# Optimization experiments

Measured on AMD Instinct MI355X. Metric: run time of the kernel, lower is better.

Reference implementation:

```python
import jax, jax.numpy as jnp
import numpy as np

N, B, F_X, F_U, H, E = 1000000, 4096, 128, 128, 64, 1024


def setup_inputs() -> dict:
    key = jax.random.key(0)
    ks = jax.random.split(key, 12)
    scale = lambda fan_in: 1.0 / np.sqrt(fan_in)
    return {
        "x": jax.random.normal(ks[0], (N, F_X), dtype=jnp.float32),
        "edge_index": jax.random.randint(ks[1], (2, E), 0, N, dtype=jnp.int64),
        "e": jax.random.normal(ks[2], (E, 16), dtype=jnp.float32),
        "u": jax.random.normal(ks[3], (B, F_U), dtype=jnp.float32),
        "batch": jnp.sort(jax.random.randint(ks[4], (N,), 0, B, dtype=jnp.int64)),
        "Wk": jax.random.uniform(ks[5], (F_X, H), jnp.float32, -scale(F_X), scale(F_X)),
        "bk": jax.random.uniform(ks[6], (H,), jnp.float32, -scale(F_X), scale(F_X)),
        "Wq": jax.random.uniform(ks[7], (F_U, H), jnp.float32, -scale(F_U), scale(F_U)),
        "bq": jax.random.uniform(ks[8], (H,), jnp.float32, -scale(F_U), scale(F_U)),
        "Wu": jax.random.uniform(ks[9], (F_X + F_U, F_U), jnp.float32, -scale(F_X + F_U), scale(F_X + F_U)),
        "bu": jax.random.uniform(ks[10], (F_U,), jnp.float32, -scale(F_X + F_U), scale(F_X + F_U)),
    }


def reference(x, edge_index, e, u, batch, Wk, bk, Wq, bq, Wu, bu):
    # edge_index and e are unpacked but unused in the original forward
    num_graphs = u.shape[0]
    k = x @ Wk + bk                       # [N, h]
    q = (u @ Wq + bq)[batch]              # [N, h] gather per node
    # per-node dot product (bmm of [N,1,h] x [N,h,1]) -> sigmoid gate [N,1]
    a = jax.nn.sigmoid(jnp.sum(k * q, axis=-1, keepdims=True))
    # gated scatter_add over batch -> [B, f_x]
    x_agg = jax.ops.segment_sum(a * x, batch, num_segments=num_graphs)
    out = jnp.concatenate([x_agg, u], axis=1)  # [B, f_x + f_u]
    return out @ Wu + bu                  # phi_u (Linear)
```

## Files before the change

kernel.cpp:

```cpp
#include <hip/hip_runtime.h>
#include <hip/hip_bf16.h>
#include <cstddef>


__global__ __launch_bounds__(64) void precompute_vc(
    const float* __restrict__ u, const float* __restrict__ Wq,
    const float* __restrict__ bq, const float* __restrict__ Wk,
    const float* __restrict__ bk, float* __restrict__ v, float* __restrict__ c) {
  const int b = blockIdx.x;
  const int h = threadIdx.x;
  __shared__ alignas(16) float us[128];
  __shared__ float qs[64];

  float2 uu = *(const float2*)(u + (size_t)b * 128 + 2 * h);
  us[2 * h] = uu.x;
  us[2 * h + 1] = uu.y;
  __syncthreads();

  float q = bq[h];
  for (int d = 0; d < 128; d += 4) {
    float4 ud = *(const float4*)&us[d];
    q = fmaf(ud.x, Wq[(d + 0) * 64 + h], q);
    q = fmaf(ud.y, Wq[(d + 1) * 64 + h], q);
    q = fmaf(ud.z, Wq[(d + 2) * 64 + h], q);
    q = fmaf(ud.w, Wq[(d + 3) * 64 + h], q);
  }
  qs[h] = q;

  float pc = q * bk[h];
#pragma unroll
  for (int m = 32; m; m >>= 1) pc += __shfl_xor(pc, m);
  if (h == 0) c[b] = pc;
  __syncthreads();

  float v0 = 0.f, v1 = 0.f;
  const float* wk0 = Wk + (size_t)h * 64;
  const float* wk1 = Wk + (size_t)(h + 64) * 64;
  for (int hh = 0; hh < 64; ++hh) {
    float qv = qs[hh];
    v0 = fmaf(qv, wk0[hh], v0);
    v1 = fmaf(qv, wk1[hh], v1);
  }
  v[(size_t)b * 128 + h] = v0;
  v[(size_t)b * 128 + 64 + h] = v1;
}

#define TPB 256
#define WPB (TPB / 64)
__global__ __launch_bounds__(TPB) void gate_scatter(
    const float* __restrict__ x, const int* __restrict__ batch,
    const float* __restrict__ v, const float* __restrict__ c,
    float* __restrict__ agg, int N, int nwaves) {
  const int wave = blockIdx.x * WPB + (threadIdx.x >> 6);
  const int lane = threadIdx.x & 63;
  const int per = (N + nwaves - 1) / nwaves;
  const int start = wave * per;
  const int end = min(N, start + per);
  if (start >= end) return;

  int curb = batch[start];
  float2 vv = *(const float2*)(v + (size_t)curb * 128 + 2 * lane);
  float cb = c[curb];
  float a0 = 0.f, a1 = 0.f;

  for (int i = start; i < end; ++i) {
    const int b = batch[i];
    if (b != curb) {
      atomicAdd(&agg[(size_t)curb * 128 + 2 * lane], a0);
      atomicAdd(&agg[(size_t)curb * 128 + 2 * lane + 1], a1);
      a0 = 0.f;
      a1 = 0.f;
      curb = b;
      vv = *(const float2*)(v + (size_t)curb * 128 + 2 * lane);
      cb = c[curb];
    }
    const float2 xx = *(const float2*)(x + (size_t)i * 128 + 2 * lane);
    float p = fmaf(xx.x, vv.x, xx.y * vv.y);
    p += __shfl_xor(p, 1);
    p += __shfl_xor(p, 2);
    p += __shfl_xor(p, 4);
    p += __shfl_xor(p, 8);
    p += __shfl_xor(p, 16);
    p += __shfl_xor(p, 32);
    const float z = p + cb;
    const float a = 1.0f / (1.0f + __expf(-z));
    a0 = fmaf(a, xx.x, a0);
    a1 = fmaf(a, xx.y, a1);
  }
  atomicAdd(&agg[(size_t)curb * 128 + 2 * lane], a0);
  atomicAdd(&agg[(size_t)curb * 128 + 2 * lane + 1], a1);
}

__global__ __launch_bounds__(128) void phi_u(
    const float* __restrict__ agg, const float* __restrict__ u,
    const float* __restrict__ Wu, const float* __restrict__ bu,
    float* __restrict__ out) {
  const int o = threadIdx.x;
  const int b0 = blockIdx.x * 8;
  __shared__ alignas(16) float s[8][256];
#pragma unroll
  for (int g = 0; g < 8; ++g) {
    s[g][o] = agg[(size_t)(b0 + g) * 128 + o];
    s[g][128 + o] = u[(size_t)(b0 + g) * 128 + o];
  }
  __syncthreads();

  float acc[8];
  const float bo = bu[o];
#pragma unroll
  for (int g = 0; g < 8; ++g) acc[g] = bo;

  for (int d = 0; d < 256; d += 4) {
    const float w0 = Wu[(size_t)(d + 0) * 128 + o];
    const float w1 = Wu[(size_t)(d + 1) * 128 + o];
    const float w2 = Wu[(size_t)(d + 2) * 128 + o];
    const float w3 = Wu[(size_t)(d + 3) * 128 + o];
#pragma unroll
    for (int g = 0; g < 8; ++g) {
      const float4 sv = *(const float4*)&s[g][d];
      acc[g] = fmaf(sv.x, w0, acc[g]);
      acc[g] = fmaf(sv.y, w1, acc[g]);
      acc[g] = fmaf(sv.z, w2, acc[g]);
      acc[g] = fmaf(sv.w, w3, acc[g]);
    }
  }
#pragma unroll
  for (int g = 0; g < 8; ++g) out[(size_t)(b0 + g) * 128 + o] = acc[g];
}

extern "C" void kernel_launch(void* const* d_in, const int* in_sizes, int n_in,
                              void* d_out, int out_size, void* d_ws, size_t ws_size,
                              hipStream_t stream) {
  const float* x = (const float*)d_in[0];
  const float* u = (const float*)d_in[3];
  const int* batch = (const int*)d_in[4];
  const float* Wk = (const float*)d_in[5];
  const float* bk = (const float*)d_in[6];
  const float* Wq = (const float*)d_in[7];
  const float* bq = (const float*)d_in[8];
  const float* Wu = (const float*)d_in[9];
  const float* bu = (const float*)d_in[10];
  float* out = (float*)d_out;

  const int N = in_sizes[0] / 128;
  const int B = in_sizes[3] / 128;

  char* ws = (char*)d_ws;
  float* v = (float*)ws;
  float* c = (float*)(ws + (size_t)B * 128 * 4);
  float* agg = (float*)(ws + (size_t)B * 128 * 4 + (size_t)B * 4);

  hipMemsetAsync(agg, 0, (size_t)B * 128 * 4, stream);

  precompute_vc<<<B, 64, 0, stream>>>(u, Wq, bq, Wk, bk, v, c);

  const int nwaves = 8192;
  gate_scatter<<<nwaves / WPB, TPB, 0, stream>>>(x, batch, v, c, agg, N, nwaves);

  phi_u<<<B / 8, 128, 0, stream>>>(agg, u, Wu, bu, out);
}
```

Baseline: 770.5 us.

## Split q/v precompute into tiled kernels and process two rows per wave in scatter

The precompute is split in two. One kernel computes q and c and also zeroes agg, which replaces the separate memset. A second kernel computes v through shared-memory tiles of Wk and q, instead of each block reading Wk with a strided, uncoalesced pattern. The gate-scatter kernel now has each half-wave handle one row with float4 loads, so a wave covers two rows per iteration, and it prefetches the next x row and batch index to hide latency. The trade-offs are one extra launch, more shared memory in kv, and per-half segment flushes triggered by a wave-wide __any check.

After: 722.7 us. -6.2%, faster.

```diff
diff --git a/kernel.cpp b/kernel.cpp
--- a/kernel.cpp
+++ b/kernel.cpp
@@ -3,92 +3,149 @@
 #include <cstddef>
 
 
-__global__ __launch_bounds__(64) void precompute_vc(
+__global__ __launch_bounds__(64) void kq(
     const float* __restrict__ u, const float* __restrict__ Wq,
-    const float* __restrict__ bq, const float* __restrict__ Wk,
-    const float* __restrict__ bk, float* __restrict__ v, float* __restrict__ c) {
+    const float* __restrict__ bq, const float* __restrict__ bk,
+    float* __restrict__ q, float* __restrict__ c, float* __restrict__ agg) {
   const int b = blockIdx.x;
   const int h = threadIdx.x;
   __shared__ alignas(16) float us[128];
-  __shared__ float qs[64];
 
   float2 uu = *(const float2*)(u + (size_t)b * 128 + 2 * h);
   us[2 * h] = uu.x;
   us[2 * h + 1] = uu.y;
   __syncthreads();
 
-  float q = bq[h];
+  float acc = bq[h];
   for (int d = 0; d < 128; d += 4) {
     float4 ud = *(const float4*)&us[d];
-    q = fmaf(ud.x, Wq[(d + 0) * 64 + h], q);
-    q = fmaf(ud.y, Wq[(d + 1) * 64 + h], q);
-    q = fmaf(ud.z, Wq[(d + 2) * 64 + h], q);
-    q = fmaf(ud.w, Wq[(d + 3) * 64 + h], q);
-  }
-  qs[h] = q;
-
-  float pc = q * bk[h];
+    acc = fmaf(ud.x, Wq[(d + 0) * 64 + h], acc);
+    acc = fmaf(ud.y, Wq[(d + 1) * 64 + h], acc);
+    acc = fmaf(ud.z, Wq[(d + 2) * 64 + h], acc);
+    acc = fmaf(ud.w, Wq[(d + 3) * 64 + h], acc);
+  }
+  q[(size_t)b * 64 + h] = acc;
+
+  float pc = acc * bk[h];
 #pragma unroll
   for (int m = 32; m; m >>= 1) pc += __shfl_xor(pc, m);
   if (h == 0) c[b] = pc;
+
+  *(float2*)(agg + (size_t)b * 128 + 2 * h) = make_float2(0.f, 0.f);
+}
+
+__global__ __launch_bounds__(128) void kv(
+    const float* __restrict__ Wk, const float* __restrict__ q,
+    float* __restrict__ v) {
+  const int t = threadIdx.x;
+  const int g0 = blockIdx.x * 16;
+  __shared__ float wk[128 * 65];
+  __shared__ alignas(16) float qs[64 * 20];
+
+  for (int j = 0; j < 16; ++j) {
+    const int idx = (j * 128 + t) * 4;
+    const float4 w4 = *(const float4*)(Wk + idx);
+    const int d = idx >> 6;
+    const int hh = idx & 63;
+    wk[d * 65 + hh + 0] = w4.x;
+    wk[d * 65 + hh + 1] = w4.y;
+    wk[d * 65 + hh + 2] = w4.z;
+    wk[d * 65 + hh + 3] = w4.w;
+  }
+  for (int j = 0; j < 8; ++j) {
+    const int idx = j * 128 + t;
+    const int g = idx >> 6;
+    const int hh = idx & 63;
+    qs[hh * 20 + g] = q[(size_t)(g0 + g) * 64 + hh];
+  }
   __syncthreads();
 
-  float v0 = 0.f, v1 = 0.f;
-  const float* wk0 = Wk + (size_t)h * 64;
-  const float* wk1 = Wk + (size_t)(h + 64) * 64;
+  const int o = t;
+  float acc[16];
+#pragma unroll
+  for (int g = 0; g < 16; ++g) acc[g] = 0.f;
+
   for (int hh = 0; hh < 64; ++hh) {
-    float qv = qs[hh];
-    v0 = fmaf(qv, wk0[hh], v0);
-    v1 = fmaf(qv, wk1[hh], v1);
-  }
-  v[(size_t)b * 128 + h] = v0;
-  v[(size_t)b * 128 + 64 + h] = v1;
+    const float w = wk[o * 65 + hh];
+    const float4 q0 = *(const float4*)&qs[hh * 20 + 0];
+    const float4 q1 = *(const float4*)&qs[hh * 20 + 4];
+    const float4 q2 = *(const float4*)&qs[hh * 20 + 8];
+    const float4 q3 = *(const float4*)&qs[hh * 20 + 12];
+    acc[0] = fmaf(w, q0.x, acc[0]);   acc[1] = fmaf(w, q0.y, acc[1]);
+    acc[2] = fmaf(w, q0.z, acc[2]);   acc[3] = fmaf(w, q0.w, acc[3]);
+    acc[4] = fmaf(w, q1.x, acc[4]);   acc[5] = fmaf(w, q1.y, acc[5]);
+    acc[6] = fmaf(w, q1.z, acc[6]);   acc[7] = fmaf(w, q1.w, acc[7]);
+    acc[8] = fmaf(w, q2.x, acc[8]);   acc[9] = fmaf(w, q2.y, acc[9]);
+    acc[10] = fmaf(w, q2.z, acc[10]); acc[11] = fmaf(w, q2.w, acc[11]);
+    acc[12] = fmaf(w, q3.x, acc[12]); acc[13] = fmaf(w, q3.y, acc[13]);
+    acc[14] = fmaf(w, q3.z, acc[14]); acc[15] = fmaf(w, q3.w, acc[15]);
+  }
+#pragma unroll
+  for (int g = 0; g < 16; ++g) v[(size_t)(g0 + g) * 128 + o] = acc[g];
 }
 
 #define TPB 256
 #define WPB (TPB / 64)
+#define PER 124
 __global__ __launch_bounds__(TPB) void gate_scatter(
     const float* __restrict__ x, const int* __restrict__ batch,
     const float* __restrict__ v, const float* __restrict__ c,
-    float* __restrict__ agg, int N, int nwaves) {
+    float* __restrict__ agg, int N) {
   const int wave = blockIdx.x * WPB + (threadIdx.x >> 6);
   const int lane = threadIdx.x & 63;
-  const int per = (N + nwaves - 1) / nwaves;
-  const int start = wave * per;
-  const int end = min(N, start + per);
-  if (start >= end) return;
-
-  int curb = batch[start];
-  float2 vv = *(const float2*)(v + (size_t)curb * 128 + 2 * lane);
+  const int half = lane >> 5;
+  const int col4 = (lane & 31) * 4;
+  const int start = wave * PER;
+  if (start >= N) return;
+  const int end = min(N, start + PER);
+
+  int idx0 = min(start + half, end - 1);
+  int bcur = batch[idx0];
+  const float* xptr = x + (size_t)(start + half) * 128 + col4;
+  float4 xx = (start + half < end) ? *(const float4*)xptr
+                                   : make_float4(0.f, 0.f, 0.f, 0.f);
+  int curb = bcur;
+  float4 vv = *(const float4*)(v + (size_t)curb * 128 + col4);
   float cb = c[curb];
-  float a0 = 0.f, a1 = 0.f;
-
-  for (int i = start; i < end; ++i) {
-    const int b = batch[i];
-    if (b != curb) {
-      atomicAdd(&agg[(size_t)curb * 128 + 2 * lane], a0);
-      atomicAdd(&agg[(size_t)curb * 128 + 2 * lane + 1], a1);
-      a0 = 0.f;
-      a1 = 0.f;
-      curb = b;
-      vv = *(const float2*)(v + (size_t)curb * 128 + 2 * lane);
+  float4 acc = make_float4(0.f, 0.f, 0.f, 0.f);
+
+  for (int i = start; i < end; i += 2) {
+    const int ni = i + 2;
+    float4 xn = make_float4(0.f, 0.f, 0.f, 0.f);
+    int bn = bcur;
+    if (ni < end) {
+      bn = batch[min(ni + half, end - 1)];
+      if (ni + half < end) xn = *(const float4*)(xptr + 256);
+    }
+    if (__any(bcur != curb)) {
+      atomicAdd(&agg[(size_t)curb * 128 + col4 + 0], acc.x);
+      atomicAdd(&agg[(size_t)curb * 128 + col4 + 1], acc.y);
+      atomicAdd(&agg[(size_t)curb * 128 + col4 + 2], acc.z);
+      atomicAdd(&agg[(size_t)curb * 128 + col4 + 3], acc.w);
+      acc = make_float4(0.f, 0.f, 0.f, 0.f);
+      curb = bcur;
+      vv = *(const float4*)(v + (size_t)curb * 128 + col4);
       cb = c[curb];
     }
-    const float2 xx = *(const float2*)(x + (size_t)i * 128 + 2 * lane);
-    float p = fmaf(xx.x, vv.x, xx.y * vv.y);
+    float p = fmaf(xx.x, vv.x, fmaf(xx.y, vv.y, fmaf(xx.z, vv.z, xx.w * vv.w)));
     p += __shfl_xor(p, 1);
     p += __shfl_xor(p, 2);
     p += __shfl_xor(p, 4);
     p += __shfl_xor(p, 8);
     p += __shfl_xor(p, 16);
-    p += __shfl_xor(p, 32);
-    const float z = p + cb;
-    const float a = 1.0f / (1.0f + __expf(-z));
-    a0 = fmaf(a, xx.x, a0);
-    a1 = fmaf(a, xx.y, a1);
-  }
-  atomicAdd(&agg[(size_t)curb * 128 + 2 * lane], a0);
-  atomicAdd(&agg[(size_t)curb * 128 + 2 * lane + 1], a1);
+    const float a = 1.0f / (1.0f + __expf(-(p + cb)));
+    acc.x = fmaf(a, xx.x, acc.x);
+    acc.y = fmaf(a, xx.y, acc.y);
+    acc.z = fmaf(a, xx.z, acc.z);
+    acc.w = fmaf(a, xx.w, acc.w);
+    xx = xn;
+    bcur = bn;
+    xptr += 256;
+  }
+  atomicAdd(&agg[(size_t)curb * 128 + col4 + 0], acc.x);
+  atomicAdd(&agg[(size_t)curb * 128 + col4 + 1], acc.y);
+  atomicAdd(&agg[(size_t)curb * 128 + col4 + 2], acc.z);
+  atomicAdd(&agg[(size_t)curb * 128 + col4 + 3], acc.w);
 }
 
 __global__ __launch_bounds__(128) void phi_u(
@@ -146,16 +203,17 @@
   const int B = in_sizes[3] / 128;
 
   char* ws = (char*)d_ws;
-  float* v = (float*)ws;
-  float* c = (float*)(ws + (size_t)B * 128 * 4);
-  float* agg = (float*)(ws + (size_t)B * 128 * 4 + (size_t)B * 4);
-
-  hipMemsetAsync(agg, 0, (size_t)B * 128 * 4, stream);
-
-  precompute_vc<<<B, 64, 0, stream>>>(u, Wq, bq, Wk, bk, v, c);
-
-  const int nwaves = 8192;
-  gate_scatter<<<nwaves / WPB, TPB, 0, stream>>>(x, batch, v, c, agg, N, nwaves);
+  float* q = (float*)ws;
+  float* v = (float*)(ws + (size_t)B * 64 * 4);
+  float* c = (float*)(ws + (size_t)B * 64 * 4 + (size_t)B * 128 * 4);
+  float* agg = (float*)(ws + (size_t)B * 64 * 4 + (size_t)B * 128 * 4 + (size_t)B * 4);
+
+  kq<<<B, 64, 0, stream>>>(u, Wq, bq, bk, q, c, agg);
+  kv<<<B / 16, 128, 0, stream>>>(Wk, q, v);
+
+  const int nwaves = (N + PER - 1) / PER;
+  const int nblocks = (nwaves + WPB - 1) / WPB;
+  gate_scatter<<<nblocks, TPB, 0, stream>>>(x, batch, v, c, agg, N);
 
   phi_u<<<B / 8, 128, 0, stream>>>(agg, u, Wu, bu, out);
 }
```
